# Kernel tuning notes

Hardware: AMD Instinct MI355X
Metric: run time of the kernel (lower is better)

## Reference

```python
import jax, jax.numpy as jnp
import numpy as np

BETA_MAX = 5.0


def setup_inputs() -> dict:
    key = jax.random.key(0)
    ks = jax.random.split(key, 10)
    N, M, R, d, NTAU, G = 100000, 1000000, 4, 16, 16, 128
    return {
        "c_3": jax.random.randint(ks[0], (M,), 0, N),
        "u_3": jax.random.randint(ks[1], (M,), 0, N),
        "v_3": jax.random.randint(ks[2], (M,), 0, N),
        "t_tau": jax.random.randint(ks[3], (M,), 0, NTAU),
        "batch": jnp.sort(jax.random.randint(ks[4], (N,), 0, G)),
        "Q3": jax.random.normal(ks[5], (N, R, d), dtype=jnp.float32),
        "K3": jax.random.normal(ks[6], (N, R, d), dtype=jnp.float32),
        "T_params": jax.random.normal(ks[7], (NTAU, d), dtype=jnp.float32),
        "raw_lambda_3": jax.random.uniform(ks[8], (1,), dtype=jnp.float32),
        "raw_beta_3": jax.random.uniform(ks[9], (1,), dtype=jnp.float32),
        "num_nodes": N,
        "num_graphs": G,
    }


def reference(c_3, u_3, v_3, t_tau, batch, Q3, K3, T_params,
              raw_lambda_3, raw_beta_3, num_nodes, num_graphs):
    R, d = Q3.shape[-2], Q3.shape[-1]
    scale = (R * d) ** 0.5
    lam = jax.nn.softplus(raw_lambda_3[0])            # positive_param
    beta = jnp.minimum(jax.nn.softplus(raw_beta_3[0]), BETA_MAX)  # inverse_temperature

    # fused motif dot: gather Q/K by triangle indices, contract over d -> [M, R]
    T_sel = T_params[t_tau]                           # [M, d]
    ell = jnp.einsum('mrd,mrd,mrd,md->mr', Q3[c_3], K3[u_3], K3[v_3], T_sel) / scale
    z = beta * ell                                    # [M, R]

    # segment logsumexp over center-node segments c_3 -> [num_nodes, R]
    seg_max = jax.ops.segment_max(z, c_3, num_segments=num_nodes)
    safe_max = jnp.where(jnp.isfinite(seg_max), seg_max, 0.0)
    sums = jax.ops.segment_sum(jnp.exp(z - safe_max[c_3]), c_3, num_segments=num_nodes)
    lse = jnp.where(sums > 0, safe_max + jnp.log(jnp.where(sums > 0, sums, 1.0)), 0.0)

    # scatter-add node lse into graphs -> [num_graphs, R]
    graph_lse = jax.ops.segment_sum(lse, batch, num_segments=num_graphs)
    return (lam / beta) * graph_lse
```

## Files before the change

kernel.cpp:

```cpp
#include <hip/hip_runtime.h>


#define RR 4
#define DD 16
#define BETA_MAX 5.0f

typedef float v2f __attribute__((ext_vector_type(2)));
typedef float v4f __attribute__((ext_vector_type(4)));

#if defined(__has_builtin)
#if __has_builtin(__builtin_nontemporal_load)
#define NT_LOAD(p) __builtin_nontemporal_load(p)
#else
#define NT_LOAD(p) (*(p))
#endif
#else
#define NT_LOAD(p) (*(p))
#endif

__device__ __forceinline__ float softplus_f(float x) {
    return log1pf(__expf(x));
}

__device__ __forceinline__ int pack4_fp8(v4f f) {
    int w = 0;
    w = __builtin_amdgcn_cvt_pk_fp8_f32(f.x, f.y, w, false);
    w = __builtin_amdgcn_cvt_pk_fp8_f32(f.z, f.w, w, true);
    return w;
}

__global__ void me_init_convert(const float* __restrict__ raw_lam,
                                const float* __restrict__ raw_beta,
                                const float* __restrict__ Q3,
                                const float* __restrict__ K3,
                                int* __restrict__ Q8, int* __restrict__ K8,
                                float* __restrict__ scal, float* __restrict__ sums,
                                float* __restrict__ out,
                                int n4each, int nr, int out_size) {
    int i = blockIdx.x * blockDim.x + threadIdx.x;
    if (i == 0) {
        float beta = fminf(softplus_f(raw_beta[0]), BETA_MAX);
        float lam  = softplus_f(raw_lam[0]);
        scal[0] = beta * 0.125f;
        scal[1] = lam / beta;
    }
    if (i < nr) sums[i] = 0.0f;
    if (i < out_size) out[i] = 0.0f;
    if (i < 2 * n4each) {
        const float* src = (i < n4each) ? Q3 : K3;
        int*         dst = (i < n4each) ? Q8 : K8;
        int j = (i < n4each) ? i : i - n4each;
        v4f f = NT_LOAD((const v4f*)src + j);
        dst[j] = pack4_fp8(f);
    }
}

__device__ __forceinline__ float dot16_fp8(int4 q8, int4 u8, int4 v8,
                                           const float* Trow) {
    float acc = 0.0f;
    const int qw[4] = {q8.x, q8.y, q8.z, q8.w};
    const int uw[4] = {u8.x, u8.y, u8.z, u8.w};
    const int vw[4] = {v8.x, v8.y, v8.z, v8.w};
#pragma unroll
    for (int j = 0; j < 4; ++j) {
        v2f ql = __builtin_amdgcn_cvt_pk_f32_fp8(qw[j], false);
        v2f qh = __builtin_amdgcn_cvt_pk_f32_fp8(qw[j], true);
        v2f ul = __builtin_amdgcn_cvt_pk_f32_fp8(uw[j], false);
        v2f uh = __builtin_amdgcn_cvt_pk_f32_fp8(uw[j], true);
        v2f vl = __builtin_amdgcn_cvt_pk_f32_fp8(vw[j], false);
        v2f vh = __builtin_amdgcn_cvt_pk_f32_fp8(vw[j], true);
        const v4f tw = *(const v4f*)(Trow + 4 * j);
        acc += ql.x * ul.x * vl.x * tw.x + ql.y * ul.y * vl.y * tw.y +
               qh.x * uh.x * vh.x * tw.z + qh.y * uh.y * vh.y * tw.w;
    }
    return acc;
}

__global__ __launch_bounds__(256)
void me_motif_8(const int* __restrict__ c3, const int* __restrict__ u3,
                const int* __restrict__ v3, const int* __restrict__ tt,
                const int4* __restrict__ Q8, const int4* __restrict__ K8,
                const float* __restrict__ Tp, const float* __restrict__ scal,
                float* __restrict__ sums, int M, int quarter) {
    __shared__ float Tl[256];
    {
        float bscale = scal[0];
        Tl[threadIdx.x] = Tp[threadIdx.x] * bscale;
    }
    __syncthreads();

    int tid = blockIdx.x * blockDim.x + threadIdx.x;
    int m0 = tid >> 2;
    if (m0 >= quarter) return;
    int k = tid & 3;

    int m1 = m0 + quarter, m2 = m0 + 2 * quarter, m3 = m0 + 3 * quarter;
    bool h1 = (m1 < M), h2 = (m2 < M), h3 = (m3 < M);
    int m1c = h1 ? m1 : m0, m2c = h2 ? m2 : m0, m3c = h3 ? m3 : m0;

    int c0 = NT_LOAD(c3 + m0),  u0 = NT_LOAD(u3 + m0);
    int v0 = NT_LOAD(v3 + m0),  t0 = NT_LOAD(tt + m0);
    int c1 = NT_LOAD(c3 + m1c), u1 = NT_LOAD(u3 + m1c);
    int v1 = NT_LOAD(v3 + m1c), t1 = NT_LOAD(tt + m1c);
    int c2 = NT_LOAD(c3 + m2c), u2 = NT_LOAD(u3 + m2c);
    int v2 = NT_LOAD(v3 + m2c), t2 = NT_LOAD(tt + m2c);
    int c3i = NT_LOAD(c3 + m3c), u3i = NT_LOAD(u3 + m3c);
    int v3i = NT_LOAD(v3 + m3c), t3 = NT_LOAD(tt + m3c);

    int4 q0 = Q8[(size_t)c0 * 4 + k];
    int4 a0 = K8[(size_t)u0 * 4 + k];
    int4 b0 = K8[(size_t)v0 * 4 + k];
    int4 q1 = Q8[(size_t)c1 * 4 + k];
    int4 a1 = K8[(size_t)u1 * 4 + k];
    int4 b1 = K8[(size_t)v1 * 4 + k];
    int4 q2 = Q8[(size_t)c2 * 4 + k];
    int4 a2 = K8[(size_t)u2 * 4 + k];
    int4 b2 = K8[(size_t)v2 * 4 + k];
    int4 q3 = Q8[(size_t)c3i * 4 + k];
    int4 a3 = K8[(size_t)u3i * 4 + k];
    int4 b3 = K8[(size_t)v3i * 4 + k];

    float p0 = dot16_fp8(q0, a0, b0, &Tl[t0 * DD]);
    float p1 = dot16_fp8(q1, a1, b1, &Tl[t1 * DD]);
    float p2 = dot16_fp8(q2, a2, b2, &Tl[t2 * DD]);
    float p3 = dot16_fp8(q3, a3, b3, &Tl[t3 * DD]);

    atomicAdd(&sums[c0 * RR + k], __expf(p0));
    if (h1) atomicAdd(&sums[c1 * RR + k], __expf(p1));
    if (h2) atomicAdd(&sums[c2 * RR + k], __expf(p2));
    if (h3) atomicAdd(&sums[c3i * RR + k], __expf(p3));
}

__global__ void me_motif_f32(const int* __restrict__ c3, const int* __restrict__ u3,
                             const int* __restrict__ v3, const int* __restrict__ tt,
                             const float* __restrict__ Q3, const float* __restrict__ K3,
                             const float* __restrict__ Tp, const float* __restrict__ scal,
                             float* __restrict__ sums, int M) {
    int tid = blockIdx.x * blockDim.x + threadIdx.x;
    int m = tid >> 4;
    if (m >= M) return;
    int l = tid & 15;
    int r = l >> 2;
    int off = r * DD + ((l & 3) << 2);
    int dc  = (l & 3) << 2;

    int c = c3[m], u = u3[m], v = v3[m], t = tt[m];
    float bscale = scal[0];

    const float4 q  = *(const float4*)(Q3 + ((size_t)c * (RR * DD) + off));
    const float4 ku = *(const float4*)(K3 + ((size_t)u * (RR * DD) + off));
    const float4 kv = *(const float4*)(K3 + ((size_t)v * (RR * DD) + off));
    const float4 tw = *(const float4*)(Tp + ((size_t)t * DD + dc));

    float p = q.x * ku.x * kv.x * tw.x + q.y * ku.y * kv.y * tw.y +
              q.z * ku.z * kv.z * tw.z + q.w * ku.w * kv.w * tw.w;
    p += __shfl_xor(p, 1);
    p += __shfl_xor(p, 2);

    if ((l & 3) == 0) atomicAdd(&sums[c * RR + r], __expf(bscale * p));
}

__global__ void me_init_f32(const float* __restrict__ raw_lam,
                            const float* __restrict__ raw_beta,
                            float* __restrict__ scal, float* __restrict__ sums,
                            float* __restrict__ out, int nr, int out_size) {
    int i = blockIdx.x * blockDim.x + threadIdx.x;
    if (i == 0) {
        float beta = fminf(softplus_f(raw_beta[0]), BETA_MAX);
        float lam  = softplus_f(raw_lam[0]);
        scal[0] = beta * 0.125f;
        scal[1] = lam / beta;
    }
    if (i < nr) sums[i] = 0.0f;
    if (i < out_size) out[i] = 0.0f;
}

__global__ void me_node(const float* __restrict__ sums, const int* __restrict__ batch,
                        const float* __restrict__ scal, float* __restrict__ out,
                        int N, int out_size) {
    extern __shared__ float acc[];
    for (int i = threadIdx.x; i < out_size; i += blockDim.x) acc[i] = 0.0f;
    __syncthreads();

    for (int n = blockIdx.x * blockDim.x + threadIdx.x; n < N;
         n += gridDim.x * blockDim.x) {
        v4f s = *((const v4f*)sums + n);
        int g = batch[n] * RR;
        if (s.x > 0.0f) atomicAdd(&acc[g + 0], logf(s.x));
        if (s.y > 0.0f) atomicAdd(&acc[g + 1], logf(s.y));
        if (s.z > 0.0f) atomicAdd(&acc[g + 2], logf(s.z));
        if (s.w > 0.0f) atomicAdd(&acc[g + 3], logf(s.w));
    }
    __syncthreads();

    float coef = scal[1];
    for (int i = threadIdx.x; i < out_size; i += blockDim.x) {
        float a = acc[i];
        if (a != 0.0f) atomicAdd(&out[i], a * coef);
    }
}

extern "C" void kernel_launch(void* const* d_in, const int* in_sizes, int n_in,
                              void* d_out, int out_size, void* d_ws, size_t ws_size,
                              hipStream_t stream) {
    const int*   c3    = (const int*)d_in[0];
    const int*   u3    = (const int*)d_in[1];
    const int*   v3    = (const int*)d_in[2];
    const int*   tt    = (const int*)d_in[3];
    const int*   batch = (const int*)d_in[4];
    const float* Q3    = (const float*)d_in[5];
    const float* K3    = (const float*)d_in[6];
    const float* Tp    = (const float*)d_in[7];
    const float* rlam  = (const float*)d_in[8];
    const float* rbeta = (const float*)d_in[9];

    const int M   = in_sizes[0];
    const int nel = in_sizes[5];
    const int N   = nel / (RR * DD);
    const int nr  = N * RR;

    const size_t fp8_bytes = (size_t)nel;
    const size_t need = 2 * fp8_bytes + (4 + (size_t)nr) * sizeof(float);

    float* out = (float*)d_out;

    if (ws_size >= need) {
        int*   Q8   = (int*)d_ws;
        int*   K8   = (int*)((char*)d_ws + fp8_bytes);
        float* scal = (float*)((char*)d_ws + 2 * fp8_bytes);
        float* sums = scal + 4;

        const int n4each = nel / 4;
        {
            int tot = 2 * n4each;
            if (nr > tot) tot = nr;
            if (out_size > tot) tot = out_size;
            me_init_convert<<<(tot + 255) / 256, 256, 0, stream>>>(
                rlam, rbeta, Q3, K3, Q8, K8, scal, sums, out, n4each, nr, out_size);
        }
        {
            const int quarter = (M + 3) / 4;
            long long threads = (long long)quarter * 4;
            int blocks = (int)((threads + 255) / 256);
            me_motif_8<<<blocks, 256, 0, stream>>>(c3, u3, v3, tt, (const int4*)Q8,
                                                   (const int4*)K8, Tp, scal, sums,
                                                   M, quarter);
        }
        {
            int nblk = (N + 255) / 256;
            if (nblk > 256) nblk = 256;
            me_node<<<nblk, 256, (size_t)out_size * sizeof(float), stream>>>(
                sums, batch, scal, out, N, out_size);
        }
    } else {
        float* scal = (float*)d_ws;
        float* sums = scal + 4;
        {
            int tot = nr > out_size ? nr : out_size;
            me_init_f32<<<(tot + 255) / 256, 256, 0, stream>>>(rlam, rbeta, scal, sums, out, nr, out_size);
        }
        {
            long long threads = (long long)M * 16;
            int blocks = (int)((threads + 255) / 256);
            me_motif_f32<<<blocks, 256, 0, stream>>>(c3, u3, v3, tt, Q3, K3, Tp, scal, sums, M);
        }
        {
            int nblk = (N + 255) / 256;
            if (nblk > 256) nblk = 256;
            me_node<<<nblk, 256, (size_t)out_size * sizeof(float), stream>>>(
                sums, batch, scal, out, N, out_size);
        }
    }
}
```

Measured before the change: 182.2 us.

## Store fp8 Q/K rank-major and split motif kernel over rank via grid y

The fp8 conversion now writes Q and K rank-major ([R][N][16 bytes]) instead of node-major. The motif kernel launches one grid slice per rank, and each thread handles two motifs for one rank, where before each thread handled four motifs with the four ranks spread across lanes. The aim is to shrink the gather working set per rank slice so it fits in cache, at the cost of reading the index arrays four times and losing the 64-byte contiguous per-node gathers.

```diff
diff --git a/kernel.cpp b/kernel.cpp
--- a/kernel.cpp
+++ b/kernel.cpp
@@ -36,7 +36,7 @@
                                 int* __restrict__ Q8, int* __restrict__ K8,
                                 float* __restrict__ scal, float* __restrict__ sums,
                                 float* __restrict__ out,
-                                int n4each, int nr, int out_size) {
+                                int n4each, int N, int nr, int out_size) {
     int i = blockIdx.x * blockDim.x + threadIdx.x;
     if (i == 0) {
         float beta = fminf(softplus_f(raw_beta[0]), BETA_MAX);
@@ -51,7 +51,10 @@
         int*         dst = (i < n4each) ? Q8 : K8;
         int j = (i < n4each) ? i : i - n4each;
         v4f f = NT_LOAD((const v4f*)src + j);
-        dst[j] = pack4_fp8(f);
+        int q = j & 3;
+        int r = (j >> 2) & 3;
+        int n = j >> 4;
+        dst[(size_t)r * N * 4 + n * 4 + q] = pack4_fp8(f);
     }
 }
 
@@ -77,58 +80,42 @@
 }
 
 __global__ __launch_bounds__(256)
-void me_motif_8(const int* __restrict__ c3, const int* __restrict__ u3,
+void me_motif_r(const int* __restrict__ c3, const int* __restrict__ u3,
                 const int* __restrict__ v3, const int* __restrict__ tt,
                 const int4* __restrict__ Q8, const int4* __restrict__ K8,
                 const float* __restrict__ Tp, const float* __restrict__ scal,
-                float* __restrict__ sums, int M, int quarter) {
+                float* __restrict__ sums, int M, int N, int halfM) {
     __shared__ float Tl[256];
-    {
-        float bscale = scal[0];
-        Tl[threadIdx.x] = Tp[threadIdx.x] * bscale;
-    }
+    Tl[threadIdx.x] = Tp[threadIdx.x] * scal[0];
     __syncthreads();
 
-    int tid = blockIdx.x * blockDim.x + threadIdx.x;
-    int m0 = tid >> 2;
-    if (m0 >= quarter) return;
-    int k = tid & 3;
-
-    int m1 = m0 + quarter, m2 = m0 + 2 * quarter, m3 = m0 + 3 * quarter;
-    bool h1 = (m1 < M), h2 = (m2 < M), h3 = (m3 < M);
-    int m1c = h1 ? m1 : m0, m2c = h2 ? m2 : m0, m3c = h3 ? m3 : m0;
+    int r = blockIdx.y;
+    const int4* Qs = Q8 + (size_t)r * N;
+    const int4* Ks = K8 + (size_t)r * N;
+
+    int m0 = blockIdx.x * blockDim.x + threadIdx.x;
+    if (m0 >= halfM) return;
+    int m1 = m0 + halfM;
+    bool h1 = (m1 < M);
+    int m1c = h1 ? m1 : m0;
 
     int c0 = NT_LOAD(c3 + m0),  u0 = NT_LOAD(u3 + m0);
     int v0 = NT_LOAD(v3 + m0),  t0 = NT_LOAD(tt + m0);
     int c1 = NT_LOAD(c3 + m1c), u1 = NT_LOAD(u3 + m1c);
     int v1 = NT_LOAD(v3 + m1c), t1 = NT_LOAD(tt + m1c);
-    int c2 = NT_LOAD(c3 + m2c), u2 = NT_LOAD(u3 + m2c);
-    int v2 = NT_LOAD(v3 + m2c), t2 = NT_LOAD(tt + m2c);
-    int c3i = NT_LOAD(c3 + m3c), u3i = NT_LOAD(u3 + m3c);
-    int v3i = NT_LOAD(v3 + m3c), t3 = NT_LOAD(tt + m3c);
-
-    int4 q0 = Q8[(size_t)c0 * 4 + k];
-    int4 a0 = K8[(size_t)u0 * 4 + k];
-    int4 b0 = K8[(size_t)v0 * 4 + k];
-    int4 q1 = Q8[(size_t)c1 * 4 + k];
-    int4 a1 = K8[(size_t)u1 * 4 + k];
-    int4 b1 = K8[(size_t)v1 * 4 + k];
-    int4 q2 = Q8[(size_t)c2 * 4 + k];
-    int4 a2 = K8[(size_t)u2 * 4 + k];
-    int4 b2 = K8[(size_t)v2 * 4 + k];
-    int4 q3 = Q8[(size_t)c3i * 4 + k];
-    int4 a3 = K8[(size_t)u3i * 4 + k];
-    int4 b3 = K8[(size_t)v3i * 4 + k];
+
+    int4 q0 = Qs[c0];
+    int4 a0 = Ks[u0];
+    int4 b0 = Ks[v0];
+    int4 q1 = Qs[c1];
+    int4 a1 = Ks[u1];
+    int4 b1 = Ks[v1];
 
     float p0 = dot16_fp8(q0, a0, b0, &Tl[t0 * DD]);
     float p1 = dot16_fp8(q1, a1, b1, &Tl[t1 * DD]);
-    float p2 = dot16_fp8(q2, a2, b2, &Tl[t2 * DD]);
-    float p3 = dot16_fp8(q3, a3, b3, &Tl[t3 * DD]);
-
-    atomicAdd(&sums[c0 * RR + k], __expf(p0));
-    if (h1) atomicAdd(&sums[c1 * RR + k], __expf(p1));
-    if (h2) atomicAdd(&sums[c2 * RR + k], __expf(p2));
-    if (h3) atomicAdd(&sums[c3i * RR + k], __expf(p3));
+
+    atomicAdd(&sums[c0 * RR + r], __expf(p0));
+    if (h1) atomicAdd(&sums[c1 * RR + r], __expf(p1));
 }
 
 __global__ void me_motif_f32(const int* __restrict__ c3, const int* __restrict__ u3,
@@ -236,15 +223,15 @@
             if (nr > tot) tot = nr;
             if (out_size > tot) tot = out_size;
             me_init_convert<<<(tot + 255) / 256, 256, 0, stream>>>(
-                rlam, rbeta, Q3, K3, Q8, K8, scal, sums, out, n4each, nr, out_size);
-        }
-        {
-            const int quarter = (M + 3) / 4;
-            long long threads = (long long)quarter * 4;
-            int blocks = (int)((threads + 255) / 256);
-            me_motif_8<<<blocks, 256, 0, stream>>>(c3, u3, v3, tt, (const int4*)Q8,
-                                                   (const int4*)K8, Tp, scal, sums,
-                                                   M, quarter);
+                rlam, rbeta, Q3, K3, Q8, K8, scal, sums, out, n4each, N, nr, out_size);
+        }
+        {
+            const int halfM = (M + 1) / 2;
+            int gx = (halfM + 255) / 256;
+            dim3 grid(gx, RR, 1);
+            me_motif_r<<<grid, 256, 0, stream>>>(c3, u3, v3, tt, (const int4*)Q8,
+                                                 (const int4*)K8, Tp, scal, sums,
+                                                 M, N, halfM);
         }
         {
             int nblk = (N + 255) / 256;
```

After: 334.3 us. +83.5%, slower.
